# Kernel optimization log

Measured on AMD Instinct MI355X. Metric: run time of the kernel, lower is better.

The kernel has to match this reference:

```python
import jax, jax.numpy as jnp
import numpy as np

K = 20
EPS = 1e-5
NEG_SLOPE = 0.2


def _graph_feature(x, k):
    # x: [B, N, C] -> edge features [B, N, k, 2C]
    xx = jnp.sum(x * x, axis=-1)                       # [B, N]
    inner = jnp.einsum('bnc,bmc->bnm', x, x)           # [B, N, N]
    neg_dist = 2.0 * inner - xx[:, :, None] - xx[:, None, :]
    idx = jax.lax.top_k(neg_dist, k)[1]                # [B, N, k] nearest neighbors
    nbr = jax.vmap(lambda f, i: f[i])(x, idx)          # [B, N, k, C]
    center = jnp.broadcast_to(x[:, :, None, :], nbr.shape)
    return jnp.concatenate([nbr - center, center], axis=-1)


def _bn(y, gamma, beta, axes):
    mu = y.mean(axes, keepdims=True)
    var = y.var(axes, keepdims=True)
    return (y - mu) * jax.lax.rsqrt(var + EPS) * gamma + beta


def _lrelu(y):
    return jnp.where(y > 0, y, NEG_SLOPE * y)


def _edge_block(feat, w, gamma, beta):
    # feat: [B, N, k, Cin], w: [Cout, Cin] (1x1 conv)
    y = jnp.einsum('bnkc,oc->bnko', feat, w)
    y = _lrelu(_bn(y, gamma, beta, (0, 1, 2)))
    return y.max(axis=2)                               # max over k -> [B, N, Cout]


def setup_inputs() -> dict:
    key = jax.random.key(0)
    ks = jax.random.split(key, 8)
    B, N = 16, 2048
    num_features = 128
    x = jax.random.normal(ks[0], (B, N, 3), dtype=jnp.float32)
    s = 0.05
    w1 = jax.random.normal(ks[1], (64, 6), dtype=jnp.float32) * s
    w2 = jax.random.normal(ks[2], (64, 128), dtype=jnp.float32) * s
    w3 = jax.random.normal(ks[3], (128, 128), dtype=jnp.float32) * s
    w4 = jax.random.normal(ks[4], (256, 256), dtype=jnp.float32) * s
    w5 = jax.random.normal(ks[5], (512, 512), dtype=jnp.float32) * s
    we = jax.random.normal(ks[6], (num_features, 512), dtype=jnp.float32) * s
    def gb(c):
        return jnp.ones((c,), jnp.float32), jnp.zeros((c,), jnp.float32)
    g1, b1 = gb(64); g2, b2 = gb(64); g3, b3 = gb(128); g4, b4 = gb(256); g5, b5 = gb(512)
    return dict(x=x, w1=w1, g1=g1, b1=b1, w2=w2, g2=g2, b2=b2, w3=w3, g3=g3, b3=b3,
                w4=w4, g4=g4, b4=b4, w5=w5, g5=g5, b5=b5, we=we)


def reference(x, w1, g1, b1, w2, g2, b2, w3, g3, b3, w4, g4, b4, w5, g5, b5, we):
    # x: [B, N, 3]
    x1 = _edge_block(_graph_feature(x, K), w1, g1, b1)    # [B, N, 64]
    x2 = _edge_block(_graph_feature(x1, K), w2, g2, b2)   # [B, N, 64]
    x3 = _edge_block(_graph_feature(x2, K), w3, g3, b3)   # [B, N, 128]
    x4 = _edge_block(_graph_feature(x3, K), w4, g4, b4)   # [B, N, 256]
    cat = jnp.concatenate([x1, x2, x3, x4], axis=-1)      # [B, N, 512]
    y = jnp.einsum('bnc,oc->bno', cat, w5)                # conv5 (1x1 conv1d)
    y = _lrelu(_bn(y, g5, b5, (0, 1)))
    y = y.max(axis=1)                                     # global max pool -> [B, 512]
    return y @ we.T                                       # embedding -> [B, num_features]
```

## Files before the change

### kernel.cpp

```cpp
#include <hip/hip_runtime.h>
#include <hip/hip_bf16.h>
#include <cstdint>

#define B_ 16
#define N_ 2048
#define KNN_K 20
#define EPS_ 1e-5f
#define SLOPE_ 0.2f
#define IMS 4.8828125e-4f

typedef __attribute__((ext_vector_type(4))) float f32x4;
typedef __attribute__((ext_vector_type(8))) short bf16x8;
typedef __attribute__((ext_vector_type(8))) _Float16 f16x8;

static __device__ __forceinline__ float lrelu(float v){ return v > 0.f ? v : SLOPE_*v; }

static __device__ __forceinline__ unsigned encf(float f){
  unsigned b = __float_as_uint(f);
  return (b & 0x80000000u) ? ~b : (b | 0x80000000u);
}
static __device__ __forceinline__ float decf(unsigned u){
  unsigned b = (u & 0x80000000u) ? (u ^ 0x80000000u) : ~u;
  return __uint_as_float(b);
}
static __device__ __forceinline__ short bfbits(float v){
  __hip_bfloat16 h = __float2bfloat16(v);
  return *reinterpret_cast<short*>(&h);
}
static __device__ __forceinline__ short h16(float v){
  _Float16 h = (_Float16)v;
  return *reinterpret_cast<short*>(&h);
}
static __device__ __forceinline__ float h2f(short s){
  _Float16 h = *reinterpret_cast<_Float16*>(&s);
  return (float)h;
}

template<int C, int CP>
__global__ __launch_bounds__(256) void convert_kernel(const float* __restrict__ f, int lda,
                                                      short* __restrict__ fbf, size_t plane,
                                                      float* __restrict__ xx){
  int wid  = (blockIdx.x * 256 + threadIdx.x) >> 6;
  int lane = threadIdx.x & 63;
  if (wid >= B_*N_) return;
  const float* p = f + (size_t)wid*lda;
  float s = 0.f;
  for (int c = lane; c < CP; c += 64){
    float v = (c < C) ? p[c] : 0.f;
    short h = h16(v);
    short m = h16((v - h2f(h)) * 2048.f);
    size_t o = (size_t)wid*CP + c;
    fbf[o] = h;
    fbf[plane + o] = m;
    s += v*v;
  }
  #pragma unroll
  for (int off=32; off; off>>=1) s += __shfl_down(s, off);
  if (lane==0) xx[wid] = s;
}

template<int CP>
__global__ __launch_bounds__(256, 2) void knn_mfma(const short* __restrict__ fbf, size_t plane,
                                                const float* __restrict__ xx,
                                                float* __restrict__ pval, int* __restrict__ pidx){
  constexpr int SP = CP + 8;
  constexpr int CH = CP/8;
  constexpr int KC = CP/32;
  constexpr int PFH = CP/32;
  constexpr int FMBS = 2*64*SP;
  constexpr bool ALIAS = (FMBS*2 >= 64*65*4);
  constexpr unsigned LDSB = ALIAS ? (unsigned)(FMBS*2) : (unsigned)(FMBS*2 + 64*65*4);
  __shared__ __align__(16) char ldsbuf[LDSB];
  short* fmb = (short*)ldsbuf;
  float* dtile = ALIAS ? (float*)ldsbuf : (float*)(ldsbuf + FMBS*2);
  __shared__ float xn_s[64], xm_s[64];

  int b   = blockIdx.x >> 6;
  int rem = blockIdx.x & 63;
  int n0  = (rem >> 1) << 6;
  int mh  = rem & 1;
  int mbase = mh << 10;
  int tid = threadIdx.x;
  int w    = tid >> 6;
  int lane = tid & 63;
  int fr = lane & 15, hi = lane >> 4;
  int r_loc = lane >> 2, csub = lane & 3;
  int gb = lane & 60;
  int myrow = w*16 + r_loc;
  size_t browoff = (size_t)b * N_;

  f16x8 aH[KC], aM[KC];
  {
    size_t arow = (browoff + n0 + w*16 + fr) * (size_t)CP;
    #pragma unroll
    for (int kc=0; kc<KC; ++kc){
      aH[kc] = *(const f16x8*)&fbf[arow + kc*32 + hi*8];
      aM[kc] = *(const f16x8*)&fbf[plane + arow + kc*32 + hi*8];
    }
  }
  if (tid < 64) xn_s[tid] = xx[browoff + n0 + tid];

  float sv[5]; int si[5];
  #pragma unroll
  for (int j=0;j<5;++j){ sv[j] = -1e30f; si[j] = 0x7FFFFFFF; }

  f16x8 pf[PFH];
  float xmreg = 0.f;
  auto PFLOAD = [&](int mt){
    int m0 = mbase + (mt<<6);
    #pragma unroll
    for (int j=0;j<PFH;++j){
      int i = tid + j*256;
      int r = i/CH, cq = i - r*CH;
      pf[j] = *(const f16x8*)&fbf[(browoff + m0 + r)*(size_t)CP + cq*8];
    }
    if (tid < 64) xmreg = xx[browoff + m0 + tid];
  };
  auto WRITEPF = [&](int mt){
    int m0 = mbase + (mt<<6);
    #pragma unroll
    for (int j=0;j<PFH;++j){
      int i = tid + j*256;
      int r = i/CH, cq = i - r*CH;
      *(f16x8*)&fmb[r*SP + cq*8] = pf[j];
    }
    #pragma unroll
    for (int j=0;j<PFH;++j){
      int i = tid + j*256;
      int r = i/CH, cq = i - r*CH;
      f16x8 v = *(const f16x8*)&fbf[plane + (browoff + m0 + r)*(size_t)CP + cq*8];
      *(f16x8*)&fmb[64*SP + r*SP + cq*8] = v;
    }
    if (tid < 64) xm_s[tid] = xmreg;
  };

  PFLOAD(0);
  WRITEPF(0);
  __syncthreads();

  for (int mt = 0; mt < 16; ++mt){
    int m0 = mbase + (mt << 6);
    if (mt + 1 < 16) PFLOAD(mt + 1);

    f32x4 accH[4], accM[4];
    #pragma unroll
    for (int ct=0; ct<4; ++ct){ accH[ct] = (f32x4){0.f,0.f,0.f,0.f}; accM[ct] = accH[ct]; }
    const short* BH = fmb;
    const short* BM = fmb + 64*SP;
    #pragma unroll
    for (int kc = 0; kc < KC; ++kc){
      #pragma unroll
      for (int ct=0; ct<4; ++ct){
        int boff = (ct*16 + fr)*SP + kc*32 + hi*8;
        f16x8 bh = *(const f16x8*)&BH[boff];
        f16x8 bm = *(const f16x8*)&BM[boff];
        accH[ct] = __builtin_amdgcn_mfma_f32_16x16x32_f16(aH[kc], bh, accH[ct], 0,0,0);
        accM[ct] = __builtin_amdgcn_mfma_f32_16x16x32_f16(aM[kc], bh, accM[ct], 0,0,0);
        accM[ct] = __builtin_amdgcn_mfma_f32_16x16x32_f16(aH[kc], bm, accM[ct], 0,0,0);
      }
    }
    __syncthreads();

    #pragma unroll
    for (int reg=0; reg<4; ++reg){
      int nl = w*16 + hi*4 + reg;
      float xn = xn_s[nl];
      #pragma unroll
      for (int ct=0; ct<4; ++ct)
        dtile[nl*65 + ct*16 + fr] = 2.f*(accH[ct][reg] + IMS*accM[ct][reg]) - xn - xm_s[ct*16 + fr];
    }

    int base = myrow*65 + csub*16;
    float thr = __shfl(sv[4], lane | 3);
    unsigned qm = 0u;
    #pragma unroll
    for (int jj=0; jj<16; ++jj){
      float v = dtile[base + jj];
      qm |= (v > thr) ? (1u << jj) : 0u;
    }
    unsigned long long bal = __ballot(qm != 0u);
    while (bal){
      unsigned nib = (unsigned)((bal >> gb) & 0xFull);
      int leader = nib ? (gb + (int)__builtin_ctz(nib)) : 64;
      int bbit = (int)__builtin_ctz(qm | 0x10000u);
      float mv = dtile[base + (bbit & 15)];
      int mid = m0 + (csub << 4) + bbit;
      float cv = __shfl(mv, leader);
      int   cid = __shfl(mid, leader);
      qm = (lane == leader) ? (qm & (qm - 1u)) : qm;
      int cnt = 0;
      #pragma unroll
      for (int j=0;j<5;++j) cnt += (sv[j] >= cv) ? 1 : 0;
      cnt += __shfl_xor(cnt, 1);
      cnt += __shfl_xor(cnt, 2);
      int pos = nib ? cnt : 20;
      float pv = __shfl_up(sv[4], 1);
      int   pi = __shfl_up(si[4], 1);
      #pragma unroll
      for (int j=0;j<5;++j){
        int g = csub*5 + j;
        float ns = (g < pos) ? sv[j] : ((g == pos) ? cv : pv);
        int   ni = (g < pos) ? si[j] : ((g == pos) ? cid : pi);
        pv = sv[j]; pi = si[j];
        sv[j] = ns; si[j] = ni;
      }
      bal = __ballot(qm != 0u);
    }

    if (mt + 1 < 16){
      if constexpr (ALIAS){
        __syncthreads();
        WRITEPF(mt + 1);
        __syncthreads();
      } else {
        WRITEPF(mt + 1);
        __syncthreads();
      }
    }
  }

  size_t orow = browoff + n0 + myrow;
  float* pvo = pval + (orow*2 + mh)*KNN_K + csub*5;
  int*   pio = pidx + (orow*2 + mh)*KNN_K + csub*5;
  #pragma unroll
  for (int j=0;j<5;++j){ pvo[j] = sv[j]; pio[j] = si[j]; }
}

__global__ __launch_bounds__(256) void knn_merge(const float* __restrict__ pval,
                                                 const int* __restrict__ pidx,
                                                 int* __restrict__ idxout){
  int r = blockIdx.x*256 + threadIdx.x;
  if (r >= B_*N_) return;
  const float* va = pval + (size_t)r*2*KNN_K;
  const float* vb = va + KNN_K;
  const int*   ia = pidx + (size_t)r*2*KNN_K;
  const int*   ib = ia + KNN_K;
  int i=0, j=0;
  #pragma unroll
  for (int t=0;t<KNN_K;++t){
    float a = va[i], bq = vb[j];
    bool ta = (a >= bq);
    idxout[(size_t)r*KNN_K + t] = ta ? ia[i] : ib[j];
    i += ta ? 1 : 0; j += ta ? 0 : 1;
  }
}

template<int CP>
__global__ __launch_bounds__(256) void gemm_pq(const short* __restrict__ fbf, size_t plane,
                                               const float* __restrict__ Wsrc, int wstride, int Cin,
                                               float* __restrict__ Out, int O){
  constexpr int BK = (CP < 64) ? CP : 64;
  constexpr int SP = BK + 8;
  __shared__ short Ah[128*SP];
  __shared__ short Am[128*SP];
  __shared__ short Wh[64*SP];
  __shared__ short Wm[64*SP];
  int obl = O >> 6;
  int bo = ((int)blockIdx.x % obl) << 6;
  int bm = ((int)blockIdx.x / obl) << 7;
  int tid = threadIdx.x;
  int w = tid >> 6, lane = tid & 63;
  int fr = lane & 15, hi = lane >> 4;
  f32x4 accH[2][4], accM[2][4];
  #pragma unroll
  for (int g=0; g<2; ++g)
    #pragma unroll
    for (int ct=0; ct<4; ++ct){ accH[g][ct] = (f32x4){0.f,0.f,0.f,0.f}; accM[g][ct] = accH[g][ct]; }

  for (int k0=0; k0<CP; k0+=BK){
    __syncthreads();
    for (int i=tid; i < 128*(BK/8); i += 256){
      int r = i/(BK/8), cq = i%(BK/8);
      size_t src = ((size_t)bm + r)*CP + k0 + cq*8;
      *(f16x8*)&Ah[r*SP + cq*8] = *(const f16x8*)&fbf[src];
      *(f16x8*)&Am[r*SP + cq*8] = *(const f16x8*)&fbf[plane + src];
    }
    for (int i=tid; i < 64*(BK/8); i += 256){
      int r = i/(BK/8), cq = i%(BK/8);
      f16x8 vh, vm;
      #pragma unroll
      for (int e=0;e<8;++e){
        int c = k0 + cq*8 + e;
        float v = (c < Cin) ? Wsrc[(size_t)(bo + r)*wstride + c] : 0.f;
        _Float16 h = (_Float16)v;
        vh[e] = h;
        vm[e] = (_Float16)((v - (float)h) * 2048.f);
      }
      *(f16x8*)&Wh[r*SP + cq*8] = vh;
      *(f16x8*)&Wm[r*SP + cq*8] = vm;
    }
    __syncthreads();
    #pragma unroll
    for (int kc=0; kc<BK/32; ++kc){
      f16x8 a0h = *(const f16x8*)&Ah[(w*32 +      fr)*SP + kc*32 + hi*8];
      f16x8 a0m = *(const f16x8*)&Am[(w*32 +      fr)*SP + kc*32 + hi*8];
      f16x8 a1h = *(const f16x8*)&Ah[(w*32 + 16 + fr)*SP + kc*32 + hi*8];
      f16x8 a1m = *(const f16x8*)&Am[(w*32 + 16 + fr)*SP + kc*32 + hi*8];
      #pragma unroll
      for (int ct=0; ct<4; ++ct){
        f16x8 bh = *(const f16x8*)&Wh[(ct*16 + fr)*SP + kc*32 + hi*8];
        f16x8 bm = *(const f16x8*)&Wm[(ct*16 + fr)*SP + kc*32 + hi*8];
        accH[0][ct] = __builtin_amdgcn_mfma_f32_16x16x32_f16(a0h, bh, accH[0][ct], 0,0,0);
        accM[0][ct] = __builtin_amdgcn_mfma_f32_16x16x32_f16(a0m, bh, accM[0][ct], 0,0,0);
        accM[0][ct] = __builtin_amdgcn_mfma_f32_16x16x32_f16(a0h, bm, accM[0][ct], 0,0,0);
        accH[1][ct] = __builtin_amdgcn_mfma_f32_16x16x32_f16(a1h, bh, accH[1][ct], 0,0,0);
        accM[1][ct] = __builtin_amdgcn_mfma_f32_16x16x32_f16(a1m, bh, accM[1][ct], 0,0,0);
        accM[1][ct] = __builtin_amdgcn_mfma_f32_16x16x32_f16(a1h, bm, accM[1][ct], 0,0,0);
      }
    }
  }
  #pragma unroll
  for (int g=0; g<2; ++g)
    #pragma unroll
    for (int ct=0; ct<4; ++ct)
      #pragma unroll
      for (int reg=0; reg<4; ++reg){
        int row = bm + w*32 + g*16 + hi*4 + reg;
        Out[(size_t)row*O + bo + ct*16 + fr] = accH[g][ct][reg] + IMS*accM[g][ct][reg];
      }
}

__global__ __launch_bounds__(256) void gemm_bf16(const float* __restrict__ A,
                                                 const float* __restrict__ Wt,
                                                 float* __restrict__ C){
  __shared__ short As[128*72];
  __shared__ short Bs[64*72];
  int bm = (int)(blockIdx.x >> 3) << 7;
  int bo = (int)(blockIdx.x & 7) << 6;
  int tid = threadIdx.x;
  int w = tid >> 6, lane = tid & 63;
  int fr = lane & 15, hi = lane >> 4;
  f32x4 acc[2][4];
  #pragma unroll
  for (int g=0; g<2; ++g)
    #pragma unroll
    for (int ct=0; ct<4; ++ct) acc[g][ct] = (f32x4){0.f,0.f,0.f,0.f};

  for (int k0=0; k0<512; k0+=64){
    __syncthreads();
    #pragma unroll 2
    for (int i = tid; i < 1024; i += 256){
      int r = i >> 3, cq = i & 7;
      const float* src = &A[(size_t)(bm + r)*512 + k0 + cq*8];
      bf16x8 v;
      #pragma unroll
      for (int e=0;e<8;++e) v[e] = bfbits(src[e]);
      *(bf16x8*)&As[r*72 + cq*8] = v;
    }
    #pragma unroll 2
    for (int i = tid; i < 512; i += 256){
      int r = i >> 3, cq = i & 7;
      const float* src = &Wt[(size_t)(bo + r)*512 + k0 + cq*8];
      bf16x8 v;
      #pragma unroll
      for (int e=0;e<8;++e) v[e] = bfbits(src[e]);
      *(bf16x8*)&Bs[r*72 + cq*8] = v;
    }
    __syncthreads();
    #pragma unroll
    for (int kc=0; kc<2; ++kc){
      bf16x8 a0 = *(const bf16x8*)&As[(w*32 +      fr)*72 + kc*32 + hi*8];
      bf16x8 a1 = *(const bf16x8*)&As[(w*32 + 16 + fr)*72 + kc*32 + hi*8];
      #pragma unroll
      for (int ct=0; ct<4; ++ct){
        bf16x8 bb = *(const bf16x8*)&Bs[(ct*16 + fr)*72 + kc*32 + hi*8];
        acc[0][ct] = __builtin_amdgcn_mfma_f32_16x16x32_bf16(a0, bb, acc[0][ct], 0,0,0);
        acc[1][ct] = __builtin_amdgcn_mfma_f32_16x16x32_bf16(a1, bb, acc[1][ct], 0,0,0);
      }
    }
  }
  #pragma unroll
  for (int g=0; g<2; ++g)
    #pragma unroll
    for (int ct=0; ct<4; ++ct)
      #pragma unroll
      for (int reg=0; reg<4; ++reg){
        int row = bm + w*32 + g*16 + hi*4 + reg;
        C[(size_t)row*512 + bo + ct*16 + fr] = acc[g][ct][reg];
      }
}

__global__ void wq_kernel(const float* __restrict__ w, float* __restrict__ wq, int Cin, int O){
  int i = blockIdx.x*blockDim.x + threadIdx.x;
  if (i >= O*Cin) return;
  int o = i / Cin, c = i - o*Cin;
  wq[i] = w[(size_t)o*2*Cin + Cin + c] - w[(size_t)o*2*Cin + c];
}

__global__ void zero_f_kernel(float* p, int n){
  int i = blockIdx.x*blockDim.x + threadIdx.x;
  if (i < n) p[i] = 0.f;
}
__global__ void zero_u_kernel(unsigned* p, int n){
  int i = blockIdx.x*blockDim.x + threadIdx.x;
  if (i < n) p[i] = 0u;
}

__global__ __launch_bounds__(256) void edge_agg(const float* __restrict__ P, const float* __restrict__ Q,
      const int* __restrict__ idx, const float* __restrict__ gamma,
      float* __restrict__ S, float* __restrict__ sums, float* __restrict__ sumsq, int O){
  const int ROWS = 64;
  int rpi = 256 / O;
  int iters = ROWS / rpi;
  int row0 = blockIdx.x * ROWS;
  int tid = threadIdx.x;
  int o  = tid % O;
  int rl = tid / O;
  int b  = row0 / N_;
  __shared__ int sidx[4][KNN_K];
  __shared__ float s1[256], s2[256];
  float g = gamma[o];
  float csum=0.f, csumsq=0.f;
  for (int it=0; it<iters; ++it){
    __syncthreads();
    if (tid < KNN_K*rpi) sidx[tid/KNN_K][tid%KNN_K] = idx[(size_t)(row0 + it*rpi)*KNN_K + tid];
    __syncthreads();
    int row = row0 + it*rpi + rl;
    float q = Q[(size_t)row*O + o];
    float mx=-1e30f, mn=1e30f, s=0.f, ss=0.f;
    #pragma unroll
    for (int k=0;k<KNN_K;++k){
      int m = sidx[rl][k];
      float p = P[((size_t)b*N_ + m)*O + o];
      mx = fmaxf(mx,p); mn = fminf(mn,p);
      float y = p + q; s += y; ss += y*y;
    }
    csum += s; csumsq += ss;
    S[(size_t)row*O + o] = (g >= 0.f ? mx : mn) + q;
  }
  s1[tid]=0.f; s2[tid]=0.f;
  __syncthreads();
  atomicAdd(&s1[o], csum); atomicAdd(&s2[o], csumsq);
  __syncthreads();
  if (tid < O){ atomicAdd(&sums[tid], s1[tid]); atomicAdd(&sumsq[tid], s2[tid]); }
}

__global__ void bn_finalize(const float* __restrict__ sums, const float* __restrict__ sumsq,
                            const float* __restrict__ gamma, const float* __restrict__ beta,
                            float invM, float* __restrict__ scale, float* __restrict__ shift, int O){
  int o = blockIdx.x*blockDim.x + threadIdx.x;
  if (o >= O) return;
  float mu = sums[o]*invM;
  float var = sumsq[o]*invM - mu*mu;
  float rs = rsqrtf(var + EPS_);
  float sc = gamma[o]*rs;
  scale[o] = sc; shift[o] = beta[o] - mu*sc;
}

__global__ void apply_write(const float* __restrict__ S, const float* __restrict__ scale,
                            const float* __restrict__ shift, float* __restrict__ cat, int off, int O){
  int i = blockIdx.x*blockDim.x + threadIdx.x;
  if (i >= B_*N_*O) return;
  int row = i / O, o = i - row*O;
  float v = S[i]*scale[o] + shift[o];
  cat[(size_t)row*512 + off + o] = lrelu(v);
}

__global__ __launch_bounds__(256) void conv5_stats(const float* __restrict__ Y, const float* __restrict__ g5,
      float* __restrict__ sums, float* __restrict__ sumsq, unsigned* __restrict__ maxenc){
  int bb = blockIdx.x / 16;
  int n0 = (blockIdx.x % 16) * 128;
  int tid = threadIdx.x;
  float s0=0.f, s1=0.f, q0=0.f, q1=0.f, m0=-1e30f, m1=-1e30f;
  float ga = g5[tid], gb = g5[tid+256];
  for (int n=0;n<128;++n){
    size_t base = ((size_t)bb*N_ + n0 + n)*512;
    float ya = Y[base + tid];
    float yb = Y[base + tid + 256];
    s0 += ya; q0 += ya*ya;
    s1 += yb; q1 += yb*yb;
    m0 = fmaxf(m0, ga>=0.f ? ya : -ya);
    m1 = fmaxf(m1, gb>=0.f ? yb : -yb);
  }
  atomicAdd(&sums[tid],      s0); atomicAdd(&sumsq[tid],      q0);
  atomicAdd(&sums[tid+256],  s1); atomicAdd(&sumsq[tid+256],  q1);
  atomicMax(&maxenc[bb*512 + tid],       encf(m0));
  atomicMax(&maxenc[bb*512 + tid + 256], encf(m1));
}

__global__ void pool_kernel(const unsigned* __restrict__ maxenc, const float* __restrict__ scale,
                            const float* __restrict__ shift, const float* __restrict__ g5,
                            float* __restrict__ pooled){
  int i = blockIdx.x*blockDim.x + threadIdx.x;
  if (i >= B_*512) return;
  int o = i & 511;
  float t = decf(maxenc[i]);
  float y = g5[o] >= 0.f ? t : -t;
  pooled[i] = lrelu(y*scale[o] + shift[o]);
}

__global__ void final_mm(const float* __restrict__ pooled, const float* __restrict__ we,
                         float* __restrict__ out){
  int i = blockIdx.x*blockDim.x + threadIdx.x;
  if (i >= B_*128) return;
  int b = i >> 7, j = i & 127;
  const float4* pp = (const float4*)(pooled + (size_t)b*512);
  const float4* wp = (const float4*)(we + (size_t)j*512);
  float s = 0.f;
  for (int c=0;c<128;++c){
    float4 a = pp[c], w = wp[c];
    s += a.x*w.x + a.y*w.y + a.z*w.z + a.w*w.w;
  }
  out[i] = s;
}

struct Ws {
  float* cat; float* P; float* Q; float* S; int* idx; float* xx;
  float* sums; float* sumsq; float* scale; float* shift;
  float* wq; unsigned* maxenc; float* pooled; short* fbf;
  float* pval; int* pidx;
};

template<int C, int CP>
static void run_layer(const Ws& W, const float* f, int lda, int O,
                      const float* w, const float* g, const float* bt,
                      int off_out, hipStream_t stream){
  const int M = B_*N_;
  size_t plane = (size_t)M*CP;
  convert_kernel<C, CP><<<M/4, 256, 0, stream>>>(f, lda, W.fbf, plane, W.xx);
  knn_mfma<CP><<<B_*(N_/64)*2, 256, 0, stream>>>(W.fbf, plane, W.xx, W.pval, W.pidx);
  knn_merge<<<(M+255)/256, 256, 0, stream>>>(W.pval, W.pidx, W.idx);
  int nwq = O*C;
  wq_kernel<<<(nwq+255)/256, 256, 0, stream>>>(w, W.wq, C, O);
  int grid = (M/128)*(O/64);
  gemm_pq<CP><<<grid, 256, 0, stream>>>(W.fbf, plane, w,    2*C, C, W.P, O);
  gemm_pq<CP><<<grid, 256, 0, stream>>>(W.fbf, plane, W.wq, C,   C, W.Q, O);
  zero_f_kernel<<<4, 256, 0, stream>>>(W.sums, 1024);
  edge_agg<<<M/64, 256, 0, stream>>>(W.P, W.Q, W.idx, g, W.S, W.sums, W.sumsq, O);
  bn_finalize<<<(O+255)/256, 256, 0, stream>>>(W.sums, W.sumsq, g, bt,
                                               1.f/((float)M*KNN_K), W.scale, W.shift, O);
  apply_write<<<(M*O+255)/256, 256, 0, stream>>>(W.S, W.scale, W.shift, W.cat, off_out, O);
}

extern "C" void kernel_launch(void* const* d_in, const int* in_sizes, int n_in,
                              void* d_out, int out_size, void* d_ws, size_t ws_size,
                              hipStream_t stream) {
  const float* x  = (const float*)d_in[0];
  const float* w1 = (const float*)d_in[1];
  const float* g1 = (const float*)d_in[2];
  const float* b1 = (const float*)d_in[3];
  const float* w2 = (const float*)d_in[4];
  const float* g2 = (const float*)d_in[5];
  const float* b2 = (const float*)d_in[6];
  const float* w3 = (const float*)d_in[7];
  const float* g3 = (const float*)d_in[8];
  const float* b3 = (const float*)d_in[9];
  const float* w4 = (const float*)d_in[10];
  const float* g4 = (const float*)d_in[11];
  const float* b4 = (const float*)d_in[12];
  const float* w5 = (const float*)d_in[13];
  const float* g5 = (const float*)d_in[14];
  const float* b5 = (const float*)d_in[15];
  const float* we = (const float*)d_in[16];

  char* ws = (char*)d_ws;
  Ws W;
  size_t off = 0;
  W.cat   = (float*)(ws + off); off += (size_t)16*2048*512*4;
  W.P     = (float*)(ws + off); off += (size_t)16*2048*256*4;
  W.Q     = (float*)(ws + off); off += (size_t)16*2048*256*4;
  W.S     = (float*)(ws + off); off += (size_t)16*2048*256*4;
  W.idx   = (int*)  (ws + off); off += (size_t)16*2048*20*4;
  W.xx    = (float*)(ws + off); off += (size_t)16*2048*4;
  W.sums  = (float*)(ws + off); off += 512*4;
  W.sumsq = (float*)(ws + off); off += 512*4;
  W.scale = (float*)(ws + off); off += 512*4;
  W.shift = (float*)(ws + off); off += 512*4;
  W.wq    = (float*)(ws + off); off += (size_t)256*128*4;
  W.maxenc= (unsigned*)(ws + off); off += (size_t)16*512*4;
  W.pooled= (float*)(ws + off); off += (size_t)16*512*4;
  W.fbf   = (short*)W.S;
  W.pval  = W.Q;
  W.pidx  = (int*)(W.Q + (size_t)2*16*2048*KNN_K);

  const int M = B_*N_;

  run_layer<3,   32>(W, x,           3,   64,  w1, g1, b1, 0,   stream);
  run_layer<64,  64>(W, W.cat,       512, 64,  w2, g2, b2, 64,  stream);
  run_layer<64,  64>(W, W.cat + 64,  512, 128, w3, g3, b3, 128, stream);
  run_layer<128,128>(W, W.cat + 128, 512, 256, w4, g4, b4, 256, stream);

  float* y5 = W.P;
  gemm_bf16<<<(M/128)*8, 256, 0, stream>>>(W.cat, w5, y5);
  zero_f_kernel<<<4, 256, 0, stream>>>(W.sums, 1024);
  zero_u_kernel<<<32, 256, 0, stream>>>(W.maxenc, 16*512);
  conv5_stats<<<B_*16, 256, 0, stream>>>(y5, g5, W.sums, W.sumsq, W.maxenc);
  bn_finalize<<<2, 256, 0, stream>>>(W.sums, W.sumsq, g5, b5, 1.f/(float)M, W.scale, W.shift, 512);
  pool_kernel<<<(16*512+255)/256, 256, 0, stream>>>(W.maxenc, W.scale, W.shift, g5, W.pooled);
  final_mm<<<(16*128+255)/256, 256, 0, stream>>>(W.pooled, we, (float*)d_out);
}
```

Measured before the change: 1.168 ms.

## Fuse P/Q GEMMs with weight diff and fold conv5 stats into GEMM epilogue

Merges the wq_kernel and the two gemm_pq launches into one gemm_pq2 that loads the A tile once and computes both P and Q. The Q weights (second half minus first half) are formed on the fly, and the M tile drops to 64 rows. The conv5 GEMM now reduces sum, sum of squares and the gamma-signed max directly from its accumulators using shuffles, shared-memory atomics and global atomics, which removes the 64MB y5 write and the separate conv5_stats read pass. In exchange there are more global atomics and a smaller M tile per block, which lowers A reuse in the P/Q GEMM.

New measurement: 1.162 ms. No clear change (-0.5%).

```diff
diff --git a/kernel.cpp b/kernel.cpp
--- a/kernel.cpp
+++ b/kernel.cpp
@@ -246,30 +246,33 @@
 }
 
 template<int CP>
-__global__ __launch_bounds__(256) void gemm_pq(const short* __restrict__ fbf, size_t plane,
-                                               const float* __restrict__ Wsrc, int wstride, int Cin,
-                                               float* __restrict__ Out, int O){
+__global__ __launch_bounds__(256) void gemm_pq2(const short* __restrict__ fbf, size_t plane,
+                                                const float* __restrict__ Wsrc, int Cin,
+                                                float* __restrict__ P, float* __restrict__ Qo, int O){
   constexpr int BK = (CP < 64) ? CP : 64;
   constexpr int SP = BK + 8;
-  __shared__ short Ah[128*SP];
-  __shared__ short Am[128*SP];
-  __shared__ short Wh[64*SP];
-  __shared__ short Wm[64*SP];
+  __shared__ short Ah[64*SP];
+  __shared__ short Am[64*SP];
+  __shared__ short WAh[64*SP];
+  __shared__ short WAm[64*SP];
+  __shared__ short WQh[64*SP];
+  __shared__ short WQm[64*SP];
   int obl = O >> 6;
   int bo = ((int)blockIdx.x % obl) << 6;
-  int bm = ((int)blockIdx.x / obl) << 7;
+  int bm = ((int)blockIdx.x / obl) << 6;
   int tid = threadIdx.x;
   int w = tid >> 6, lane = tid & 63;
   int fr = lane & 15, hi = lane >> 4;
-  f32x4 accH[2][4], accM[2][4];
-  #pragma unroll
-  for (int g=0; g<2; ++g)
-    #pragma unroll
-    for (int ct=0; ct<4; ++ct){ accH[g][ct] = (f32x4){0.f,0.f,0.f,0.f}; accM[g][ct] = accH[g][ct]; }
+  f32x4 aPH[4], aPM[4], aQH[4], aQM[4];
+  #pragma unroll
+  for (int ct=0; ct<4; ++ct){
+    aPH[ct] = (f32x4){0.f,0.f,0.f,0.f};
+    aPM[ct] = aPH[ct]; aQH[ct] = aPH[ct]; aQM[ct] = aPH[ct];
+  }
 
   for (int k0=0; k0<CP; k0+=BK){
     __syncthreads();
-    for (int i=tid; i < 128*(BK/8); i += 256){
+    for (int i=tid; i < 64*(BK/8); i += 256){
       int r = i/(BK/8), cq = i%(BK/8);
       size_t src = ((size_t)bm + r)*CP + k0 + cq*8;
       *(f16x8*)&Ah[r*SP + cq*8] = *(const f16x8*)&fbf[src];
@@ -277,54 +280,68 @@
     }
     for (int i=tid; i < 64*(BK/8); i += 256){
       int r = i/(BK/8), cq = i%(BK/8);
-      f16x8 vh, vm;
+      f16x8 vah, vam, vqh, vqm;
       #pragma unroll
       for (int e=0;e<8;++e){
         int c = k0 + cq*8 + e;
-        float v = (c < Cin) ? Wsrc[(size_t)(bo + r)*wstride + c] : 0.f;
-        _Float16 h = (_Float16)v;
-        vh[e] = h;
-        vm[e] = (_Float16)((v - (float)h) * 2048.f);
-      }
-      *(f16x8*)&Wh[r*SP + cq*8] = vh;
-      *(f16x8*)&Wm[r*SP + cq*8] = vm;
+        float wa = 0.f, wqv = 0.f;
+        if (c < Cin){
+          wa  = Wsrc[(size_t)(bo + r)*2*Cin + c];
+          wqv = Wsrc[(size_t)(bo + r)*2*Cin + Cin + c] - wa;
+        }
+        _Float16 ha = (_Float16)wa;
+        vah[e] = ha;
+        vam[e] = (_Float16)((wa - (float)ha) * 2048.f);
+        _Float16 hq = (_Float16)wqv;
+        vqh[e] = hq;
+        vqm[e] = (_Float16)((wqv - (float)hq) * 2048.f);
+      }
+      *(f16x8*)&WAh[r*SP + cq*8] = vah;
+      *(f16x8*)&WAm[r*SP + cq*8] = vam;
+      *(f16x8*)&WQh[r*SP + cq*8] = vqh;
+      *(f16x8*)&WQm[r*SP + cq*8] = vqm;
     }
     __syncthreads();
     #pragma unroll
     for (int kc=0; kc<BK/32; ++kc){
-      f16x8 a0h = *(const f16x8*)&Ah[(w*32 +      fr)*SP + kc*32 + hi*8];
-      f16x8 a0m = *(const f16x8*)&Am[(w*32 +      fr)*SP + kc*32 + hi*8];
-      f16x8 a1h = *(const f16x8*)&Ah[(w*32 + 16 + fr)*SP + kc*32 + hi*8];
-      f16x8 a1m = *(const f16x8*)&Am[(w*32 + 16 + fr)*SP + kc*32 + hi*8];
+      f16x8 ah = *(const f16x8*)&Ah[(w*16 + fr)*SP + kc*32 + hi*8];
+      f16x8 am = *(const f16x8*)&Am[(w*16 + fr)*SP + kc*32 + hi*8];
       #pragma unroll
       for (int ct=0; ct<4; ++ct){
-        f16x8 bh = *(const f16x8*)&Wh[(ct*16 + fr)*SP + kc*32 + hi*8];
-        f16x8 bm = *(const f16x8*)&Wm[(ct*16 + fr)*SP + kc*32 + hi*8];
-        accH[0][ct] = __builtin_amdgcn_mfma_f32_16x16x32_f16(a0h, bh, accH[0][ct], 0,0,0);
-        accM[0][ct] = __builtin_amdgcn_mfma_f32_16x16x32_f16(a0m, bh, accM[0][ct], 0,0,0);
-        accM[0][ct] = __builtin_amdgcn_mfma_f32_16x16x32_f16(a0h, bm, accM[0][ct], 0,0,0);
-        accH[1][ct] = __builtin_amdgcn_mfma_f32_16x16x32_f16(a1h, bh, accH[1][ct], 0,0,0);
-        accM[1][ct] = __builtin_amdgcn_mfma_f32_16x16x32_f16(a1m, bh, accM[1][ct], 0,0,0);
-        accM[1][ct] = __builtin_amdgcn_mfma_f32_16x16x32_f16(a1h, bm, accM[1][ct], 0,0,0);
-      }
-    }
-  }
-  #pragma unroll
-  for (int g=0; g<2; ++g)
-    #pragma unroll
-    for (int ct=0; ct<4; ++ct)
-      #pragma unroll
-      for (int reg=0; reg<4; ++reg){
-        int row = bm + w*32 + g*16 + hi*4 + reg;
-        Out[(size_t)row*O + bo + ct*16 + fr] = accH[g][ct][reg] + IMS*accM[g][ct][reg];
-      }
-}
-
-__global__ __launch_bounds__(256) void gemm_bf16(const float* __restrict__ A,
-                                                 const float* __restrict__ Wt,
-                                                 float* __restrict__ C){
+        int boff = (ct*16 + fr)*SP + kc*32 + hi*8;
+        f16x8 bh = *(const f16x8*)&WAh[boff];
+        f16x8 bm = *(const f16x8*)&WAm[boff];
+        f16x8 qh = *(const f16x8*)&WQh[boff];
+        f16x8 qm = *(const f16x8*)&WQm[boff];
+        aPH[ct] = __builtin_amdgcn_mfma_f32_16x16x32_f16(ah, bh, aPH[ct], 0,0,0);
+        aPM[ct] = __builtin_amdgcn_mfma_f32_16x16x32_f16(am, bh, aPM[ct], 0,0,0);
+        aPM[ct] = __builtin_amdgcn_mfma_f32_16x16x32_f16(ah, bm, aPM[ct], 0,0,0);
+        aQH[ct] = __builtin_amdgcn_mfma_f32_16x16x32_f16(ah, qh, aQH[ct], 0,0,0);
+        aQM[ct] = __builtin_amdgcn_mfma_f32_16x16x32_f16(am, qh, aQM[ct], 0,0,0);
+        aQM[ct] = __builtin_amdgcn_mfma_f32_16x16x32_f16(ah, qm, aQM[ct], 0,0,0);
+      }
+    }
+  }
+  #pragma unroll
+  for (int ct=0; ct<4; ++ct)
+    #pragma unroll
+    for (int reg=0; reg<4; ++reg){
+      int row = bm + w*16 + hi*4 + reg;
+      size_t o = (size_t)row*O + bo + ct*16 + fr;
+      P[o]  = aPH[ct][reg] + IMS*aPM[ct][reg];
+      Qo[o] = aQH[ct][reg] + IMS*aQM[ct][reg];
+    }
+}
+
+__global__ __launch_bounds__(256) void gemm_bf16_stats(const float* __restrict__ A,
+                                                       const float* __restrict__ Wt,
+                                                       const float* __restrict__ g5,
+                                                       float* __restrict__ sums,
+                                                       float* __restrict__ sumsq,
+                                                       unsigned* __restrict__ maxenc){
   __shared__ short As[128*72];
   __shared__ short Bs[64*72];
+  __shared__ float s1[64], s2[64];
   int bm = (int)(blockIdx.x >> 3) << 7;
   int bo = (int)(blockIdx.x & 7) << 6;
   int tid = threadIdx.x;
@@ -369,22 +386,39 @@
       }
     }
   }
-  #pragma unroll
-  for (int g=0; g<2; ++g)
-    #pragma unroll
-    for (int ct=0; ct<4; ++ct)
+
+  __syncthreads();
+  if (tid < 64){ s1[tid] = 0.f; s2[tid] = 0.f; }
+  __syncthreads();
+  int bidx = bm >> 11;
+  #pragma unroll
+  for (int ct=0; ct<4; ++ct){
+    int o = bo + ct*16 + fr;
+    float ga = g5[o];
+    float s = 0.f, ss = 0.f, mx = -1e30f;
+    #pragma unroll
+    for (int g=0; g<2; ++g)
       #pragma unroll
       for (int reg=0; reg<4; ++reg){
-        int row = bm + w*32 + g*16 + hi*4 + reg;
-        C[(size_t)row*512 + bo + ct*16 + fr] = acc[g][ct][reg];
-      }
-}
-
-__global__ void wq_kernel(const float* __restrict__ w, float* __restrict__ wq, int Cin, int O){
-  int i = blockIdx.x*blockDim.x + threadIdx.x;
-  if (i >= O*Cin) return;
-  int o = i / Cin, c = i - o*Cin;
-  wq[i] = w[(size_t)o*2*Cin + Cin + c] - w[(size_t)o*2*Cin + c];
+        float v = acc[g][ct][reg];
+        s += v; ss += v*v;
+        float sel = ga >= 0.f ? v : -v;
+        mx = fmaxf(mx, sel);
+      }
+    s  += __shfl_xor(s, 16);  s  += __shfl_xor(s, 32);
+    ss += __shfl_xor(ss, 16); ss += __shfl_xor(ss, 32);
+    mx = fmaxf(mx, __shfl_xor(mx, 16)); mx = fmaxf(mx, __shfl_xor(mx, 32));
+    if (hi == 0){
+      atomicAdd(&s1[ct*16 + fr], s);
+      atomicAdd(&s2[ct*16 + fr], ss);
+      atomicMax(&maxenc[bidx*512 + o], encf(mx));
+    }
+  }
+  __syncthreads();
+  if (tid < 64){
+    atomicAdd(&sums[bo + tid],  s1[tid]);
+    atomicAdd(&sumsq[bo + tid], s2[tid]);
+  }
 }
 
 __global__ void zero_f_kernel(float* p, int n){
@@ -456,28 +490,6 @@
   cat[(size_t)row*512 + off + o] = lrelu(v);
 }
 
-__global__ __launch_bounds__(256) void conv5_stats(const float* __restrict__ Y, const float* __restrict__ g5,
-      float* __restrict__ sums, float* __restrict__ sumsq, unsigned* __restrict__ maxenc){
-  int bb = blockIdx.x / 16;
-  int n0 = (blockIdx.x % 16) * 128;
-  int tid = threadIdx.x;
-  float s0=0.f, s1=0.f, q0=0.f, q1=0.f, m0=-1e30f, m1=-1e30f;
-  float ga = g5[tid], gb = g5[tid+256];
-  for (int n=0;n<128;++n){
-    size_t base = ((size_t)bb*N_ + n0 + n)*512;
-    float ya = Y[base + tid];
-    float yb = Y[base + tid + 256];
-    s0 += ya; q0 += ya*ya;
-    s1 += yb; q1 += yb*yb;
-    m0 = fmaxf(m0, ga>=0.f ? ya : -ya);
-    m1 = fmaxf(m1, gb>=0.f ? yb : -yb);
-  }
-  atomicAdd(&sums[tid],      s0); atomicAdd(&sumsq[tid],      q0);
-  atomicAdd(&sums[tid+256],  s1); atomicAdd(&sumsq[tid+256],  q1);
-  atomicMax(&maxenc[bb*512 + tid],       encf(m0));
-  atomicMax(&maxenc[bb*512 + tid + 256], encf(m1));
-}
-
 __global__ void pool_kernel(const unsigned* __restrict__ maxenc, const float* __restrict__ scale,
                             const float* __restrict__ shift, const float* __restrict__ g5,
                             float* __restrict__ pooled){
@@ -507,7 +519,7 @@
 struct Ws {
   float* cat; float* P; float* Q; float* S; int* idx; float* xx;
   float* sums; float* sumsq; float* scale; float* shift;
-  float* wq; unsigned* maxenc; float* pooled; short* fbf;
+  unsigned* maxenc; float* pooled; short* fbf;
   float* pval; int* pidx;
 };
 
@@ -520,11 +532,8 @@
   convert_kernel<C, CP><<<M/4, 256, 0, stream>>>(f, lda, W.fbf, plane, W.xx);
   knn_mfma<CP><<<B_*(N_/64)*2, 256, 0, stream>>>(W.fbf, plane, W.xx, W.pval, W.pidx);
   knn_merge<<<(M+255)/256, 256, 0, stream>>>(W.pval, W.pidx, W.idx);
-  int nwq = O*C;
-  wq_kernel<<<(nwq+255)/256, 256, 0, stream>>>(w, W.wq, C, O);
-  int grid = (M/128)*(O/64);
-  gemm_pq<CP><<<grid, 256, 0, stream>>>(W.fbf, plane, w,    2*C, C, W.P, O);
-  gemm_pq<CP><<<grid, 256, 0, stream>>>(W.fbf, plane, W.wq, C,   C, W.Q, O);
+  int grid = (M/64)*(O/64);
+  gemm_pq2<CP><<<grid, 256, 0, stream>>>(W.fbf, plane, w, C, W.P, W.Q, O);
   zero_f_kernel<<<4, 256, 0, stream>>>(W.sums, 1024);
   edge_agg<<<M/64, 256, 0, stream>>>(W.P, W.Q, W.idx, g, W.S, W.sums, W.sumsq, O);
   bn_finalize<<<(O+255)/256, 256, 0, stream>>>(W.sums, W.sumsq, g, bt,
@@ -566,7 +575,6 @@
   W.sumsq = (float*)(ws + off); off += 512*4;
   W.scale = (float*)(ws + off); off += 512*4;
   W.shift = (float*)(ws + off); off += 512*4;
-  W.wq    = (float*)(ws + off); off += (size_t)256*128*4;
   W.maxenc= (unsigned*)(ws + off); off += (size_t)16*512*4;
   W.pooled= (float*)(ws + off); off += (size_t)16*512*4;
   W.fbf   = (short*)W.S;
@@ -580,11 +588,9 @@
   run_layer<64,  64>(W, W.cat + 64,  512, 128, w3, g3, b3, 128, stream);
   run_layer<128,128>(W, W.cat + 128, 512, 256, w4, g4, b4, 256, stream);
 
-  float* y5 = W.P;
-  gemm_bf16<<<(M/128)*8, 256, 0, stream>>>(W.cat, w5, y5);
   zero_f_kernel<<<4, 256, 0, stream>>>(W.sums, 1024);
   zero_u_kernel<<<32, 256, 0, stream>>>(W.maxenc, 16*512);
-  conv5_stats<<<B_*16, 256, 0, stream>>>(y5, g5, W.sums, W.sumsq, W.maxenc);
+  gemm_bf16_stats<<<(M/128)*8, 256, 0, stream>>>(W.cat, w5, g5, W.sums, W.sumsq, W.maxenc);
   bn_finalize<<<2, 256, 0, stream>>>(W.sums, W.sumsq, g5, b5, 1.f/(float)M, W.scale, W.shift, 512);
   pool_kernel<<<(16*512+255)/256, 256, 0, stream>>>(W.maxenc, W.scale, W.shift, g5, W.pooled);
   final_mm<<<(16*128+255)/256, 256, 0, stream>>>(W.pooled, we, (float*)d_out);
```
